# Performance work log

Measured on AMD Instinct MI355X. Metric: run time of the kernel, lower is better.

The kernel has to match this reference:

```python
import jax, jax.numpy as jnp
import numpy as np

B, T, K = 128, 4096, 64
START, STOP = 62, 63
NEG = -10000.0


def setup_inputs() -> dict:
    key = jax.random.key(0)
    k1, k2, k3 = jax.random.split(key, 3)
    feats = jax.random.normal(k1, (B, T, K), dtype=jnp.float32)
    # gold tags never include START/STOP
    tags = jax.random.randint(k2, (B, T), 0, START)
    transitions = jax.random.normal(k3, (K, K), dtype=jnp.float32)
    # mirror the torch __init__ masking: no transition INTO start, none OUT of stop
    transitions = transitions.at[START, :].set(NEG).at[:, STOP].set(NEG)
    return {"feats": feats, "tags": tags, "transitions": transitions}


def _crf_single(feats, tags, transitions):
    """feats: [T,K], tags: [T], transitions: [K,K] (trans[next, prev])."""
    init = jnp.full((K,), NEG, dtype=feats.dtype).at[START].set(0.0)

    # ---- forward algorithm (log partition), vectorized over the tag loop ----
    def fwd_step(alpha, feat):
        # alpha[i] + trans[j, i] + feat[j]  ->  logsumexp over prev i
        new = jax.nn.logsumexp(alpha[None, :] + transitions, axis=1) + feat
        return new, None

    alpha, _ = jax.lax.scan(fwd_step, init, feats)
    forward_score = jax.nn.logsumexp(alpha + transitions[STOP])

    # ---- gold path score (_score_session) ----
    prev_tags = jnp.concatenate([jnp.array([START], dtype=tags.dtype), tags[:-1]])
    emit = jnp.take_along_axis(feats, tags[:, None], axis=1)[:, 0]  # feats[t, tags[t]]
    gold_score = jnp.sum(transitions[tags, prev_tags] + emit) + transitions[STOP, tags[-1]]

    nll = forward_score - gold_score  # neg_log_likelihood

    # ---- Viterbi decode ----
    def vit_step(delta, feat):
        scores = delta[None, :] + transitions  # [next, prev]
        bp = jnp.argmax(scores, axis=1)
        new = jnp.max(scores, axis=1) + feat  # feat added after argmax, as in torch
        return new, bp

    delta, bps = jax.lax.scan(vit_step, init, feats)  # bps: [T, K]
    terminal = delta + transitions[STOP]
    best_last = jnp.argmax(terminal)
    path_score = terminal[best_last]

    def back_step(tag, bp_t):
        return bp_t[tag], tag

    _, best_path = jax.lax.scan(back_step, best_last, bps, reverse=True)  # [T]
    return nll, path_score, best_path


def reference(feats, tags, transitions):
    nll, path_score, best_path = jax.vmap(_crf_single, in_axes=(0, 0, None))(
        feats, tags, transitions
    )
    return nll, path_score, best_path
```

## Files before the change

### kernel.cpp

```cpp
#include <hip/hip_runtime.h>

namespace {
constexpr int Tn = 4096;
constexpr int Kn = 64;
constexpr int BATCH = 128;
constexpr int START_TAG = 62;
constexpr int STOP_TAG = 63;
constexpr float NEGV = -10000.0f;
constexpr int CH = 64;
constexpr int NCH = Tn / CH;
constexpr int GL = 8;
constexpr int NG = Tn / GL;
constexpr int RS = 128;
constexpr int RB = 128;
constexpr int CW = 16;

__device__ __forceinline__ float rfl(float x) {
    return __uint_as_float(__builtin_amdgcn_readfirstlane(__float_as_uint(x)));
}
__device__ __forceinline__ void cfence() { __asm__ volatile("" ::: "memory"); }
__device__ __forceinline__ void lgkm0() { __asm__ volatile("s_waitcnt lgkmcnt(0)" ::: "memory"); }
__device__ __forceinline__ int imin(int a, int b) { return a < b ? a : b; }

__global__ __launch_bounds__(256, 1)
void crf_kernel(const float* __restrict__ feats,
                const int* __restrict__ tags,
                const float* __restrict__ trans,
                float* __restrict__ out,
                unsigned int* __restrict__ bp32)
{
    const int tid = threadIdx.x;
    const int lane = tid & 63;
    const int wid = tid >> 6;
    const int b = blockIdx.x & (BATCH - 1);
    const size_t fb = (size_t)b * Tn * Kn;

    __shared__ float gw[4];
    __shared__ __align__(16) float vb[2][Kn];
    __shared__ __align__(16) float ring_v[RS][Kn];
    __shared__ unsigned char ring_bp[RB][Kn];
    __shared__ unsigned char snap[NCH * Kn];
    __shared__ unsigned char echain[NCH];
    __shared__ int prog_a[Kn], prog_b[Kn], prog_c[Kn], prog_d[Kn];
    __shared__ int done_b[Kn], done_c[Kn];

    if (blockIdx.x < BATCH) {
        float gold = 0.0f;
        {
            const int t0 = tid * (Tn / 256);
            int prev = (tid == 0) ? START_TAG : tags[(size_t)b * Tn + t0 - 1];
            for (int k = 0; k < Tn / 256; ++k) {
                const int t = t0 + k;
                const int tg = tags[(size_t)b * Tn + t];
                gold += trans[tg * Kn + prev] + feats[fb + (size_t)t * Kn + tg];
                prev = tg;
            }
            if (tid == 255) gold += trans[STOP_TAG * Kn + prev];
            #pragma unroll
            for (int off = 32; off; off >>= 1) gold += __shfl_down(gold, off);
            if (lane == 0) gw[wid] = gold;
        }
        __syncthreads();
        if (wid != 0) return;

        float ES[Kn];
        #pragma unroll
        for (int q = 0; q < Kn / 4; ++q) {
            const float4 t4 = ((const float4*)(trans + lane * Kn))[q];
            ES[4*q+0] = __expf(t4.x); ES[4*q+1] = __expf(t4.y);
            ES[4*q+2] = __expf(t4.z); ES[4*q+3] = __expf(t4.w);
        }
        float v = (lane == START_TAG) ? 1.0f : 0.0f;
        float O = 0.0f;
        float fc[GL], fn[GL], Fc[GL];
        #pragma unroll
        for (int k = 0; k < GL; ++k) fc[k] = feats[fb + (size_t)k * Kn + lane];

        float4 rv0[16], rv1[16];
        vb[0][lane] = v;
        {
            const float4* p0 = (const float4*)vb[0];
            #pragma unroll
            for (int q = 0; q < 16; ++q) rv0[q] = p0[q];
        }

#define FWD_STEP(RV, RN, NB, K)  do {                                          \
        float wq_[4];                                                          \
        _Pragma("unroll")                                                      \
        for (int q = 0; q < 4; ++q) {                                          \
            const float4 v0 = (RV)[4*q+0], v1 = (RV)[4*q+1],                   \
                         v2 = (RV)[4*q+2], v3 = (RV)[4*q+3];                   \
            float s0 = 0.f, s1 = 0.f, s2 = 0.f, s3 = 0.f;                      \
            s0 = fmaf(ES[16*q+0],  v0.x, s0); s1 = fmaf(ES[16*q+1],  v0.y, s1);\
            s2 = fmaf(ES[16*q+2],  v0.z, s2); s3 = fmaf(ES[16*q+3],  v0.w, s3);\
            s0 = fmaf(ES[16*q+4],  v1.x, s0); s1 = fmaf(ES[16*q+5],  v1.y, s1);\
            s2 = fmaf(ES[16*q+6],  v1.z, s2); s3 = fmaf(ES[16*q+7],  v1.w, s3);\
            s0 = fmaf(ES[16*q+8],  v2.x, s0); s1 = fmaf(ES[16*q+9],  v2.y, s1);\
            s2 = fmaf(ES[16*q+10], v2.z, s2); s3 = fmaf(ES[16*q+11], v2.w, s3);\
            s0 = fmaf(ES[16*q+12], v3.x, s0); s1 = fmaf(ES[16*q+13], v3.y, s1);\
            s2 = fmaf(ES[16*q+14], v3.z, s2); s3 = fmaf(ES[16*q+15], v3.w, s3);\
            wq_[q] = (s0 + s1) + (s2 + s3);                                    \
        }                                                                      \
        const float w_ = ((wq_[0] + wq_[1]) + (wq_[2] + wq_[3])) * Fc[K];      \
        const float wz_ = rfl(w_);                                             \
        v = w_ * __builtin_amdgcn_rcpf(wz_);                                   \
        (NB)[lane] = v;                                                        \
        const float4* np_ = (const float4*)(NB);                               \
        _Pragma("unroll")                                                      \
        for (int q = 0; q < 16; ++q) (RN)[q] = np_[q];                         \
        O += __logf(wz_);                                                      \
    } while (0)

        for (int g = 0; g < NG; ++g) {
            if (g + 1 < NG) {
                const size_t base = fb + (size_t)(g + 1) * GL * Kn + lane;
                #pragma unroll
                for (int k = 0; k < GL; ++k) fn[k] = feats[base + (size_t)k * Kn];
            }
            #pragma unroll
            for (int k = 0; k < GL; ++k) Fc[k] = __expf(fc[k]);
            #pragma unroll
            for (int k = 0; k < GL; ++k) {
                if ((k & 1) == 0) FWD_STEP(rv0, rv1, vb[1], k);
                else              FWD_STEP(rv1, rv0, vb[0], k);
            }
            #pragma unroll
            for (int k = 0; k < GL; ++k) fc[k] = fn[k];
        }
#undef FWD_STEP
        {
            const float a = O + __logf(v);
            const float x = a + trans[STOP_TAG * Kn + lane];
            float mx = x;
            #pragma unroll
            for (int off = 32; off; off >>= 1) mx = fmaxf(mx, __shfl_xor(mx, off));
            float se = __expf(x - mx);
            #pragma unroll
            for (int off = 32; off; off >>= 1) se += __shfl_xor(se, off);
            if (lane == 0)
                out[b] = (mx + __logf(se)) - (((gw[0] + gw[1]) + (gw[2] + gw[3])));
        }
        return;
    }

    volatile int* pa = (volatile int*)prog_a;
    volatile int* pb = (volatile int*)prog_b;
    volatile int* pc = (volatile int*)prog_c;
    volatile int* pd = (volatile int*)prog_d;
    volatile int* db = (volatile int*)done_b;
    volatile int* dc = (volatile int*)done_c;
    if (wid == 0) { pa[lane] = 0; pb[lane] = 0; }
    if (wid == 1) { pc[lane] = 0; pd[lane] = 0; }
    if (wid == 2) { db[lane] = 0; dc[lane] = 0; }
    __syncthreads();

    float trS[Kn];
    #pragma unroll
    for (int q = 0; q < Kn / 4; ++q) {
        const float4 t4 = ((const float4*)(trans + lane * Kn))[q];
        trS[4*q+0] = t4.x; trS[4*q+1] = t4.y; trS[4*q+2] = t4.z; trS[4*q+3] = t4.w;
    }

    if (wid == 0) {
        float v = (lane == START_TAG) ? 0.0f : NEGV;
        float fc[GL], fn[GL];
        #pragma unroll
        for (int k = 0; k < GL; ++k) fc[k] = feats[fb + (size_t)k * Kn + lane];

        float4 rv0[16], rv1[16];
        ring_v[0][lane] = v;
        {
            const float4* p0 = (const float4*)ring_v[0];
            #pragma unroll
            for (int q = 0; q < 16; ++q) rv0[q] = p0[q];
        }

#define VIT_STEP(RV, RN, K)  do {                                              \
        const int t_ = g * GL + (K);                                           \
        float qm_[16];                                                         \
        _Pragma("unroll")                                                      \
        for (int q = 0; q < 16; ++q) {                                         \
            const float4 dv = (RV)[q];                                         \
            const float sx = dv.x + trS[4*q+0];                                \
            const float sy = dv.y + trS[4*q+1];                                \
            const float sz = dv.z + trS[4*q+2];                                \
            const float sw = dv.w + trS[4*q+3];                                \
            qm_[q] = fmaxf(fmaxf(sx, sy), fmaxf(sz, sw));                      \
        }                                                                      \
        float m8_[8];                                                          \
        _Pragma("unroll")                                                      \
        for (int q = 0; q < 8; ++q) m8_[q] = fmaxf(qm_[2*q], qm_[2*q+1]);      \
        const float mm = fmaxf(fmaxf(fmaxf(m8_[0], m8_[1]), fmaxf(m8_[2], m8_[3])), \
                               fmaxf(fmaxf(m8_[4], m8_[5]), fmaxf(m8_[6], m8_[7]))); \
        v = mm + fc[K];                  \
        float* nb_ = ring_v[(t_ + 1) & (RS - 1)];                              \
        nb_[lane] = v;                                                         \
        const float4* np_ = (const float4*)nb_;                                \
        _Pragma("unroll")                                                      \
        for (int q = 0; q < 16; ++q) (RN)[q] = np_[q];                         \
        cfence();                                                              \
        pa[lane] = t_ + 1;                \
    } while (0)

        for (int g = 0; g < NG; ++g) {
            if (g + 1 < NG) {
                const size_t base = fb + (size_t)(g + 1) * GL * Kn + lane;
                #pragma unroll
                for (int k = 0; k < GL; ++k) fn[k] = feats[base + (size_t)k * Kn];
            }
            if ((g & 3) == 0 && g >= 16) {
                const int t0 = g * GL;
                cfence();
                while (pb[lane] < t0 - 88 || pc[lane] < t0 - 88)
                    __builtin_amdgcn_s_sleep(1);
                cfence();
            }
            #pragma unroll
            for (int k = 0; k < GL; ++k) {
                if ((k & 1) == 0) VIT_STEP(rv0, rv1, k);
                else              VIT_STEP(rv1, rv0, k);
            }
            #pragma unroll
            for (int k = 0; k < GL; ++k) fc[k] = fn[k];
        }
#undef VIT_STEP
        const float term = v + trans[STOP_TAG * Kn + lane];
        float bv = term;
        int bi = lane;
        #pragma unroll
        for (int off = 32; off; off >>= 1) {
            const float ov = __shfl_xor(bv, off);
            const int oi = __shfl_xor(bi, off);
            if (ov > bv || (ov == bv && oi < bi)) { bv = ov; bi = oi; }
        }
        if (lane == 0) out[BATCH + b] = bv;
        while (pd[lane] < Tn) __builtin_amdgcn_s_sleep(1);
        cfence();
        if (lane == 0) {
            int e = bi;
            for (int c = NCH - 1; c >= 0; --c) {
                echain[c] = (unsigned char)e;
                e = snap[c * Kn + e];
            }
        }
        lgkm0();
        while (db[lane] == 0 || dc[lane] == 0) __builtin_amdgcn_s_sleep(1);
        cfence();
        int tag = echain[lane];
        float* po = out + 2 * BATCH + (size_t)b * Tn;
        const size_t dwb = (size_t)b * (Tn / 4);
        for (int k = CH - 1; k >= 0; --k) {
            const int t = lane * CH + k;
            po[t] = (float)tag;
            tag = (int)((bp32[(dwb + (size_t)(t >> 2)) * Kn + tag] >> (8 * (t & 3))) & 63u);
        }
    } else if (wid == 1 || wid == 2) {
        const int par = wid - 1;
        const size_t dwb = (size_t)b * (Tn / 4);
        volatile int* my = (par == 0) ? pb : pc;
        for (int c0 = par * CW; c0 < Tn; c0 += 2 * CW) {
            while (pa[lane] < c0 + CW) __builtin_amdgcn_s_sleep(1);
            cfence();
            if (c0 >= RB) {
                while (pd[lane] < c0 - (RB - CW)) __builtin_amdgcn_s_sleep(1);
                cfence();
            }
            for (int k4 = 0; k4 < CW; k4 += 4) {
                unsigned int bp4 = 0;
                #pragma unroll
                for (int k = 0; k < 4; ++k) {
                    const int t = c0 + k4 + k;
                    const float4* vp = (const float4*)ring_v[t & (RS - 1)];
                    float sa[64], qm[16];
                    #pragma unroll
                    for (int q = 0; q < 16; ++q) {
                        const float4 dv = vp[q];
                        sa[4*q+0] = dv.x + trS[4*q+0];
                        sa[4*q+1] = dv.y + trS[4*q+1];
                        sa[4*q+2] = dv.z + trS[4*q+2];
                        sa[4*q+3] = dv.w + trS[4*q+3];
                        qm[q] = fmaxf(fmaxf(sa[4*q+0], sa[4*q+1]),
                                      fmaxf(sa[4*q+2], sa[4*q+3]));
                    }
                    float m8[8];
                    #pragma unroll
                    for (int q = 0; q < 8; ++q) m8[q] = fmaxf(qm[2*q], qm[2*q+1]);
                    const float m = fmaxf(fmaxf(fmaxf(m8[0], m8[1]), fmaxf(m8[2], m8[3])),
                                          fmaxf(fmaxf(m8[4], m8[5]), fmaxf(m8[6], m8[7])));
                    int qi[16];
                    #pragma unroll
                    for (int q = 0; q < 16; ++q) {
                        const int i0 = 4 * q;
                        const int ix = (sa[i0+0] == m) ? i0+0 : 255;
                        const int iy = (sa[i0+1] == m) ? i0+1 : 255;
                        const int iz = (sa[i0+2] == m) ? i0+2 : 255;
                        const int iw = (sa[i0+3] == m) ? i0+3 : 255;
                        qi[q] = imin(imin(ix, iy), imin(iz, iw));
                    }
                    int i8[8];
                    #pragma unroll
                    for (int q = 0; q < 8; ++q) i8[q] = imin(qi[2*q], qi[2*q+1]);
                    const int idx = imin(imin(imin(i8[0], i8[1]), imin(i8[2], i8[3])),
                                         imin(imin(i8[4], i8[5]), imin(i8[6], i8[7])));
                    ring_bp[t & (RB - 1)][lane] = (unsigned char)idx;
                    bp4 |= (unsigned int)idx << (8 * k);
                }
                bp32[(dwb + (size_t)((c0 + k4) >> 2)) * Kn + lane] = bp4;
            }
            cfence();
            my[lane] = c0 + CW;
        }
        __asm__ volatile("s_waitcnt vmcnt(0)" ::: "memory");
        if (par == 0) db[lane] = 1; else dc[lane] = 1;
    } else {
        int h = lane;
        for (int c0 = 0; c0 < Tn; c0 += CW) {
            volatile int* pp = ((c0 >> 4) & 1) ? pc : pb;
            while (pp[lane] < c0 + CW) __builtin_amdgcn_s_sleep(1);
            cfence();
            int bpv[CW];
            #pragma unroll
            for (int k = 0; k < CW; ++k)
                bpv[k] = (int)ring_bp[(c0 + k) & (RB - 1)][lane];
            #pragma unroll
            for (int k = 0; k < CW; ++k) h = __shfl(h, bpv[k]);
            if (((c0 >> 4) & 3) == 3) {
                snap[(c0 >> 6) * Kn + lane] = (unsigned char)h;
                h = lane;
            }
            cfence();
            pd[lane] = c0 + CW;
        }
    }
}
}

extern "C" void kernel_launch(void* const* d_in, const int* in_sizes, int n_in,
                              void* d_out, int out_size, void* d_ws, size_t ws_size,
                              hipStream_t stream)
{
    const float* feats = (const float*)d_in[0];
    const int* tags   = (const int*)d_in[1];
    const float* trans = (const float*)d_in[2];
    float* out = (float*)d_out;
    unsigned int* bp = (unsigned int*)d_ws;
    hipLaunchKernelGGL(crf_kernel, dim3(2 * BATCH), dim3(256), 0, stream,
                       feats, tags, trans, out, bp);
}
```

Before: 1.812 ms.

## Pass Viterbi max to argmax waves via LDS ring and batch progress updates

```diff
diff --git a/kernel.cpp b/kernel.cpp
--- a/kernel.cpp
+++ b/kernel.cpp
@@ -21,6 +21,9 @@
 __device__ __forceinline__ void cfence() { __asm__ volatile("" ::: "memory"); }
 __device__ __forceinline__ void lgkm0() { __asm__ volatile("s_waitcnt lgkmcnt(0)" ::: "memory"); }
 __device__ __forceinline__ int imin(int a, int b) { return a < b ? a : b; }
+__device__ __forceinline__ float m3(float a, float b, float c) {
+    return fmaxf(fmaxf(a, b), c);
+}
 
 __global__ __launch_bounds__(256, 1)
 void crf_kernel(const float* __restrict__ feats,
@@ -36,13 +39,22 @@
     const size_t fb = (size_t)b * Tn * Kn;
 
     __shared__ float gw[4];
-    __shared__ __align__(16) float vb[2][Kn];
+    __shared__ __align__(16) float vbuf[Kn];
     __shared__ __align__(16) float ring_v[RS][Kn];
+    __shared__ float ring_m[RS][Kn];
     __shared__ unsigned char ring_bp[RB][Kn];
     __shared__ unsigned char snap[NCH * Kn];
     __shared__ unsigned char echain[NCH];
     __shared__ int prog_a[Kn], prog_b[Kn], prog_c[Kn], prog_d[Kn];
     __shared__ int done_b[Kn], done_c[Kn];
+
+#define GATHER16(BASE) do {                                                    \
+        const float4* vp_ = (const float4*)(BASE);                             \
+        g0 = vp_[0];  g1 = vp_[1];  g2 = vp_[2];  g3 = vp_[3];                 \
+        g4 = vp_[4];  g5 = vp_[5];  g6 = vp_[6];  g7 = vp_[7];                 \
+        g8 = vp_[8];  g9 = vp_[9];  g10 = vp_[10]; g11 = vp_[11];              \
+        g12 = vp_[12]; g13 = vp_[13]; g14 = vp_[14]; g15 = vp_[15];            \
+    } while (0)
 
     if (blockIdx.x < BATCH) {
         float gold = 0.0f;
@@ -76,39 +88,33 @@
         #pragma unroll
         for (int k = 0; k < GL; ++k) fc[k] = feats[fb + (size_t)k * Kn + lane];
 
-        float4 rv0[16], rv1[16];
-        vb[0][lane] = v;
-        {
-            const float4* p0 = (const float4*)vb[0];
-            #pragma unroll
-            for (int q = 0; q < 16; ++q) rv0[q] = p0[q];
-        }
-
-#define FWD_STEP(RV, RN, NB, K)  do {                                          \
-        float wq_[4];                                                          \
-        _Pragma("unroll")                                                      \
-        for (int q = 0; q < 4; ++q) {                                          \
-            const float4 v0 = (RV)[4*q+0], v1 = (RV)[4*q+1],                   \
-                         v2 = (RV)[4*q+2], v3 = (RV)[4*q+3];                   \
-            float s0 = 0.f, s1 = 0.f, s2 = 0.f, s3 = 0.f;                      \
-            s0 = fmaf(ES[16*q+0],  v0.x, s0); s1 = fmaf(ES[16*q+1],  v0.y, s1);\
-            s2 = fmaf(ES[16*q+2],  v0.z, s2); s3 = fmaf(ES[16*q+3],  v0.w, s3);\
-            s0 = fmaf(ES[16*q+4],  v1.x, s0); s1 = fmaf(ES[16*q+5],  v1.y, s1);\
-            s2 = fmaf(ES[16*q+6],  v1.z, s2); s3 = fmaf(ES[16*q+7],  v1.w, s3);\
-            s0 = fmaf(ES[16*q+8],  v2.x, s0); s1 = fmaf(ES[16*q+9],  v2.y, s1);\
-            s2 = fmaf(ES[16*q+10], v2.z, s2); s3 = fmaf(ES[16*q+11], v2.w, s3);\
-            s0 = fmaf(ES[16*q+12], v3.x, s0); s1 = fmaf(ES[16*q+13], v3.y, s1);\
-            s2 = fmaf(ES[16*q+14], v3.z, s2); s3 = fmaf(ES[16*q+15], v3.w, s3);\
-            wq_[q] = (s0 + s1) + (s2 + s3);                                    \
-        }                                                                      \
-        const float w_ = ((wq_[0] + wq_[1]) + (wq_[2] + wq_[3])) * Fc[K];      \
+        float4 g0, g1, g2, g3, g4, g5, g6, g7, g8, g9, g10, g11, g12, g13, g14, g15;
+        vbuf[lane] = v;
+        GATHER16(vbuf);
+
+#define FMAQ(Q, A, B2, C, D) ({                                                \
+        float s0_ = 0.f, s1_ = 0.f, s2_ = 0.f, s3_ = 0.f;                      \
+        s0_ = fmaf(ES[16*(Q)+0],  (A).x,  s0_); s1_ = fmaf(ES[16*(Q)+1],  (A).y,  s1_); \
+        s2_ = fmaf(ES[16*(Q)+2],  (A).z,  s2_); s3_ = fmaf(ES[16*(Q)+3],  (A).w,  s3_); \
+        s0_ = fmaf(ES[16*(Q)+4],  (B2).x, s0_); s1_ = fmaf(ES[16*(Q)+5],  (B2).y, s1_); \
+        s2_ = fmaf(ES[16*(Q)+6],  (B2).z, s2_); s3_ = fmaf(ES[16*(Q)+7],  (B2).w, s3_); \
+        s0_ = fmaf(ES[16*(Q)+8],  (C).x,  s0_); s1_ = fmaf(ES[16*(Q)+9],  (C).y,  s1_); \
+        s2_ = fmaf(ES[16*(Q)+10], (C).z,  s2_); s3_ = fmaf(ES[16*(Q)+11], (C).w,  s3_); \
+        s0_ = fmaf(ES[16*(Q)+12], (D).x,  s0_); s1_ = fmaf(ES[16*(Q)+13], (D).y,  s1_); \
+        s2_ = fmaf(ES[16*(Q)+14], (D).z,  s2_); s3_ = fmaf(ES[16*(Q)+15], (D).w,  s3_); \
+        (s0_ + s1_) + (s2_ + s3_); })
+
+#define FWD_STEP(K) do {                                                       \
+        const float w0_ = FMAQ(0, g0,  g1,  g2,  g3);                          \
+        const float w1_ = FMAQ(1, g4,  g5,  g6,  g7);                          \
+        const float w2_ = FMAQ(2, g8,  g9,  g10, g11);                         \
+        const float w3_ = FMAQ(3, g12, g13, g14, g15);                         \
+        const float w_ = ((w0_ + w1_) + (w2_ + w3_)) * Fc[K];                  \
         const float wz_ = rfl(w_);                                             \
         v = w_ * __builtin_amdgcn_rcpf(wz_);                                   \
-        (NB)[lane] = v;                                                        \
-        const float4* np_ = (const float4*)(NB);                               \
-        _Pragma("unroll")                                                      \
-        for (int q = 0; q < 16; ++q) (RN)[q] = np_[q];                         \
-        O += __logf(wz_);                                                      \
+        vbuf[lane] = v;                                                        \
+        GATHER16(vbuf);                 \
+        O += __logf(wz_);                   \
     } while (0)
 
         for (int g = 0; g < NG; ++g) {
@@ -120,10 +126,7 @@
             #pragma unroll
             for (int k = 0; k < GL; ++k) Fc[k] = __expf(fc[k]);
             #pragma unroll
-            for (int k = 0; k < GL; ++k) {
-                if ((k & 1) == 0) FWD_STEP(rv0, rv1, vb[1], k);
-                else              FWD_STEP(rv1, rv0, vb[0], k);
-            }
+            for (int k = 0; k < GL; ++k) FWD_STEP(k);
             #pragma unroll
             for (int k = 0; k < GL; ++k) fc[k] = fn[k];
         }
@@ -167,39 +170,38 @@
         #pragma unroll
         for (int k = 0; k < GL; ++k) fc[k] = feats[fb + (size_t)k * Kn + lane];
 
-        float4 rv0[16], rv1[16];
+        float4 g0, g1, g2, g3, g4, g5, g6, g7, g8, g9, g10, g11, g12, g13, g14, g15;
         ring_v[0][lane] = v;
-        {
-            const float4* p0 = (const float4*)ring_v[0];
-            #pragma unroll
-            for (int q = 0; q < 16; ++q) rv0[q] = p0[q];
-        }
-
-#define VIT_STEP(RV, RN, K)  do {                                              \
+        GATHER16(ring_v[0]);
+
+#define VQ(Q, DV) ({                                                           \
+        const float sx_ = (DV).x + trS[4*(Q)+0];                               \
+        const float sy_ = (DV).y + trS[4*(Q)+1];                               \
+        const float sz_ = (DV).z + trS[4*(Q)+2];                               \
+        const float sw_ = (DV).w + trS[4*(Q)+3];                               \
+        fmaxf(m3(sx_, sy_, sz_), sw_); })
+
+#define VIT_STEP(K) do {                                                       \
         const int t_ = g * GL + (K);                                           \
-        float qm_[16];                                                         \
-        _Pragma("unroll")                                                      \
-        for (int q = 0; q < 16; ++q) {                                         \
-            const float4 dv = (RV)[q];                                         \
-            const float sx = dv.x + trS[4*q+0];                                \
-            const float sy = dv.y + trS[4*q+1];                                \
-            const float sz = dv.z + trS[4*q+2];                                \
-            const float sw = dv.w + trS[4*q+3];                                \
-            qm_[q] = fmaxf(fmaxf(sx, sy), fmaxf(sz, sw));                      \
-        }                                                                      \
-        float m8_[8];                                                          \
-        _Pragma("unroll")                                                      \
-        for (int q = 0; q < 8; ++q) m8_[q] = fmaxf(qm_[2*q], qm_[2*q+1]);      \
-        const float mm = fmaxf(fmaxf(fmaxf(m8_[0], m8_[1]), fmaxf(m8_[2], m8_[3])), \
-                               fmaxf(fmaxf(m8_[4], m8_[5]), fmaxf(m8_[6], m8_[7]))); \
-        v = mm + fc[K];                  \
+        const float q0_  = VQ(0,  g0),  q1_  = VQ(1,  g1);                     \
+        const float q2_  = VQ(2,  g2),  q3_  = VQ(3,  g3);                     \
+        const float q4_  = VQ(4,  g4),  q5_  = VQ(5,  g5);                     \
+        const float q6_  = VQ(6,  g6),  q7_  = VQ(7,  g7);                     \
+        const float q8_  = VQ(8,  g8),  q9_  = VQ(9,  g9);                     \
+        const float q10_ = VQ(10, g10), q11_ = VQ(11, g11);                    \
+        const float q12_ = VQ(12, g12), q13_ = VQ(13, g13);                    \
+        const float q14_ = VQ(14, g14), q15_ = VQ(15, g15);                    \
+        const float r0_ = m3(q0_,  q1_,  q2_);                                 \
+        const float r1_ = m3(q3_,  q4_,  q5_);                                 \
+        const float r2_ = m3(q6_,  q7_,  q8_);                                 \
+        const float r3_ = m3(q9_,  q10_, q11_);                                \
+        const float r4_ = m3(q12_, q13_, q14_);                                \
+        const float mm_ = fmaxf(m3(m3(r0_, r1_, r2_), r3_, r4_), q15_);        \
+        v = mm_ + fc[K];                 \
         float* nb_ = ring_v[(t_ + 1) & (RS - 1)];                              \
         nb_[lane] = v;                                                         \
-        const float4* np_ = (const float4*)nb_;                                \
-        _Pragma("unroll")                                                      \
-        for (int q = 0; q < 16; ++q) (RN)[q] = np_[q];                         \
-        cfence();                                                              \
-        pa[lane] = t_ + 1;                \
+        GATHER16(nb_);                   \
+        ring_m[t_ & (RS - 1)][lane] = mm_;             \
     } while (0)
 
         for (int g = 0; g < NG; ++g) {
@@ -216,14 +218,14 @@
                 cfence();
             }
             #pragma unroll
-            for (int k = 0; k < GL; ++k) {
-                if ((k & 1) == 0) VIT_STEP(rv0, rv1, k);
-                else              VIT_STEP(rv1, rv0, k);
-            }
+            for (int k = 0; k < GL; ++k) VIT_STEP(k);
+            cfence();
+            pa[lane] = g * GL + GL;
             #pragma unroll
             for (int k = 0; k < GL; ++k) fc[k] = fn[k];
         }
 #undef VIT_STEP
+#undef VQ
         const float term = v + trans[STOP_TAG * Kn + lane];
         float bv = term;
         int bi = lane;
@@ -271,30 +273,19 @@
                 for (int k = 0; k < 4; ++k) {
                     const int t = c0 + k4 + k;
                     const float4* vp = (const float4*)ring_v[t & (RS - 1)];
-                    float sa[64], qm[16];
+                    const float m = ring_m[t & (RS - 1)][lane];
+                    int qi[16];
                     #pragma unroll
                     for (int q = 0; q < 16; ++q) {
                         const float4 dv = vp[q];
-                        sa[4*q+0] = dv.x + trS[4*q+0];
-                        sa[4*q+1] = dv.y + trS[4*q+1];
-                        sa[4*q+2] = dv.z + trS[4*q+2];
-                        sa[4*q+3] = dv.w + trS[4*q+3];
-                        qm[q] = fmaxf(fmaxf(sa[4*q+0], sa[4*q+1]),
-                                      fmaxf(sa[4*q+2], sa[4*q+3]));
-                    }
-                    float m8[8];
-                    #pragma unroll
-                    for (int q = 0; q < 8; ++q) m8[q] = fmaxf(qm[2*q], qm[2*q+1]);
-                    const float m = fmaxf(fmaxf(fmaxf(m8[0], m8[1]), fmaxf(m8[2], m8[3])),
-                                          fmaxf(fmaxf(m8[4], m8[5]), fmaxf(m8[6], m8[7])));
-                    int qi[16];
-                    #pragma unroll
-                    for (int q = 0; q < 16; ++q) {
-                        const int i0 = 4 * q;
-                        const int ix = (sa[i0+0] == m) ? i0+0 : 255;
-                        const int iy = (sa[i0+1] == m) ? i0+1 : 255;
-                        const int iz = (sa[i0+2] == m) ? i0+2 : 255;
-                        const int iw = (sa[i0+3] == m) ? i0+3 : 255;
+                        const float sx = dv.x + trS[4*q+0];
+                        const float sy = dv.y + trS[4*q+1];
+                        const float sz = dv.z + trS[4*q+2];
+                        const float sw = dv.w + trS[4*q+3];
+                        const int ix = (sx == m) ? 4*q+0 : 255;
+                        const int iy = (sy == m) ? 4*q+1 : 255;
+                        const int iz = (sz == m) ? 4*q+2 : 255;
+                        const int iw = (sw == m) ? 4*q+3 : 255;
                         qi[q] = imin(imin(ix, iy), imin(iz, iw));
                     }
                     int i8[8];
@@ -332,6 +323,8 @@
             pd[lane] = c0 + CW;
         }
     }
+#undef GATHER16
+#undef FMAQ
 }
 }
 
```

Result: faster. 1.684 ms (-7.1%).
